# Kernel optimization log

Measured on AMD Instinct MI355X. Metric: run time of the kernel, lower is better.

The kernel has to match this reference:

```python
import jax, jax.numpy as jnp
import numpy as np

NUM_SPECIES = 7
B, A, F = 1024, 48, 384


def setup_inputs() -> dict:
    key = jax.random.key(0)
    ks = jax.random.split(key, 10)
    species = jax.random.randint(ks[0], (B, A), 0, NUM_SPECIES, dtype=jnp.int32)
    aev = jax.random.normal(ks[1], (B, A, F), dtype=jnp.float32)
    def w(k, shape, fan_in):
        s = 1.0 / np.sqrt(fan_in).astype(np.float32)
        return jax.random.uniform(k, shape, jnp.float32, -s, s)
    return {
        "species": species,
        "aev": aev,
        "W1": w(ks[2], (NUM_SPECIES, 256, 384), 384),
        "b1": w(ks[3], (NUM_SPECIES, 256), 384),
        "W2": w(ks[4], (NUM_SPECIES, 192, 256), 256),
        "b2": w(ks[5], (NUM_SPECIES, 192), 256),
        "W3": w(ks[6], (NUM_SPECIES, 160, 192), 192),
        "b3": w(ks[7], (NUM_SPECIES, 160), 192),
        "W4": w(ks[8], (NUM_SPECIES, 1, 160), 160),
        "b4": w(ks[9], (NUM_SPECIES, 1), 160),
    }


def reference(species, aev, W1, b1, W2, b2, W3, b3, W4, b4):
    # species: [B, A] int, aev: [B, A, 384]
    celu = lambda x: jax.nn.celu(x, alpha=0.1)

    def expert(s):
        # Per-species MLP 384->256->192->160->1 applied to all atoms; selected via mask.
        h = celu(jnp.einsum('baf,hf->bah', aev, W1[s]) + b1[s])
        h = celu(jnp.einsum('bah,gh->bag', h, W2[s]) + b2[s])
        h = celu(jnp.einsum('bag,eg->bae', h, W3[s]) + b3[s])
        return (jnp.einsum('bae,oe->bao', h, W4[s]) + b4[s])[..., 0]  # [B, A]

    atom_energy = jnp.zeros(species.shape, aev.dtype)
    for s in range(NUM_SPECIES):  # fixed small expert loop (hard routing)
        atom_energy = jnp.where(species == s, expert(s), atom_energy)
    # scatter-sum atomic energies into per-molecule energies
    return atom_energy.sum(axis=1)  # [B]
```

## Files before the change

kernel.cpp:

```cpp
#include <hip/hip_runtime.h>
#include <math.h>

#define NSPEC 7
#define NMOL 1024
#define APM 48
#define NATOMS (NMOL * APM)
#define FDIM 384

typedef unsigned short u16;
typedef unsigned int u32;
typedef __attribute__((ext_vector_type(8))) short short8;
typedef __attribute__((ext_vector_type(4))) float floatx4;

#define W1_ELEMS_PER_S (16 * 12 * 64 * 8)
#define W2_ELEMS_PER_S (12 * 8 * 64 * 8)
#define W3_ELEMS_PER_S (10 * 6 * 64 * 8)
#define T1 (NSPEC * 16 * 12 * 64)
#define T2 (NSPEC * 12 * 8 * 64)
#define T3 (NSPEC * 10 * 6 * 64)
#define BUCKET_BLOCKS (NATOMS / 256)
#define PACK_BLOCKS ((T1 + T2 + T3) / 256)

#define WS_W1_OFF 32
#define WS_W2_OFF (WS_W1_OFF + 1376256)
#define WS_W3_OFF (WS_W2_OFF + 688128)
#define WS_BKT_OFF (WS_W3_OFF + 430080)

#define BUFST 264

__device__ __forceinline__ float celu01(float x) {
    return x > 0.0f ? x : 0.1f * expm1f(x * 10.0f);
}

__device__ __forceinline__ u16 bfr(float f) {
    u32 u = __float_as_uint(f);
    u += 0x7fffu + ((u >> 16) & 1u);
    return (u16)(u >> 16);
}

__device__ __forceinline__ float bf2f(short s) {
    return __uint_as_float(((u32)(u16)s) << 16);
}

union U8 { short8 v; u16 u[8]; };

__global__ void prep_kernel(const int* __restrict__ species,
                            int* __restrict__ g_cnt, u16* __restrict__ bucket,
                            const float* __restrict__ W1, const float* __restrict__ W2,
                            const float* __restrict__ W3,
                            u16* __restrict__ w1p, u16* __restrict__ w2p,
                            u16* __restrict__ w3p) {
    int t = threadIdx.x;
    if (blockIdx.x < BUCKET_BLOCKS) {
        __shared__ int l_cnt[NSPEC];
        __shared__ int l_base[NSPEC];
        if (t < NSPEC) l_cnt[t] = 0;
        __syncthreads();
        int i = blockIdx.x * 256 + t;
        int s = species[i];
        int lpos = atomicAdd(&l_cnt[s], 1);
        __syncthreads();
        if (t < NSPEC) l_base[t] = atomicAdd(&g_cnt[t], l_cnt[t]);
        __syncthreads();
        bucket[s * NATOMS + l_base[s] + lpos] = (u16)i;
    } else {
        int tid = (blockIdx.x - BUCKET_BLOCKS) * 256 + t;
        const float* W;
        u16* dst;
        int KGS, NTILES, idx;
        if (tid < T1) { W = W1; dst = w1p; KGS = 12; NTILES = 16; idx = tid; }
        else if (tid < T1 + T2) { W = W2; dst = w2p; KGS = 8; NTILES = 12; idx = tid - T1; }
        else { W = W3; dst = w3p; KGS = 6; NTILES = 10; idx = tid - (T1 + T2); }
        int lane = idx & 63;
        int q = idx >> 6;
        int kg = q % KGS; q /= KGS;
        int t2 = q % NTILES;
        int s = q / NTILES;
        int K = KGS * 32;
        int n = t2 * 16 + (lane & 15);
        int k0 = kg * 32 + ((lane >> 4) & 3) * 8;
        const float* src = W + (size_t)(s * NTILES * 16 + n) * K + k0;
        U8 x;
#pragma unroll
        for (int j = 0; j < 8; ++j) x.u[j] = bfr(src[j]);
        *reinterpret_cast<short8*>(dst + (size_t)idx * 8) = x.v;
    }
}

template <int KGS, int NTILES>
__device__ __forceinline__ void run_layer(const short8* af0, const short8* af1,
                                          const u16* __restrict__ wsp,
                                          const float* __restrict__ bias,
                                          u16* __restrict__ outbuf, int lane) {
    const int nl = lane & 15, kg4 = lane >> 4;
    short8 bcur[KGS], bnext[KGS];
    {
        const u16* wb = wsp + (size_t)lane * 8;
#pragma unroll
        for (int kg = 0; kg < KGS; ++kg)
            bcur[kg] = *reinterpret_cast<const short8*>(wb + kg * 512);
    }
#pragma unroll
    for (int t = 0; t < NTILES; ++t) {
        if (t + 1 < NTILES) {
            const u16* wb = wsp + (size_t)((t + 1) * KGS) * 512 + (size_t)lane * 8;
#pragma unroll
            for (int kg = 0; kg < KGS; ++kg)
                bnext[kg] = *reinterpret_cast<const short8*>(wb + kg * 512);
        }
        floatx4 acc0 = {0.f, 0.f, 0.f, 0.f};
        floatx4 acc1 = {0.f, 0.f, 0.f, 0.f};
#pragma unroll
        for (int kg = 0; kg < KGS; ++kg) {
            acc0 = __builtin_amdgcn_mfma_f32_16x16x32_bf16(af0[kg], bcur[kg], acc0, 0, 0, 0);
            acc1 = __builtin_amdgcn_mfma_f32_16x16x32_bf16(af1[kg], bcur[kg], acc1, 0, 0, 0);
        }
        float bn = bias[t * 16 + nl];
#pragma unroll
        for (int r = 0; r < 4; ++r) {
            outbuf[(kg4 * 4 + r) * BUFST + t * 16 + nl] = bfr(celu01(acc0[r] + bn));
            outbuf[(16 + kg4 * 4 + r) * BUFST + t * 16 + nl] = bfr(celu01(acc1[r] + bn));
        }
#pragma unroll
        for (int kg = 0; kg < KGS; ++kg) bcur[kg] = bnext[kg];
    }
}

template <int KGS>
__device__ __forceinline__ void load_a_lds(const u16* __restrict__ buf,
                                           short8* af0, short8* af1, int lane) {
    int nl = lane & 15, kg4 = lane >> 4;
#pragma unroll
    for (int kg = 0; kg < KGS; ++kg) {
        af0[kg] = *reinterpret_cast<const short8*>(buf + (size_t)nl * BUFST + kg * 32 + kg4 * 8);
        af1[kg] = *reinterpret_cast<const short8*>(buf + (size_t)(16 + nl) * BUFST + kg * 32 + kg4 * 8);
    }
}

__global__ __launch_bounds__(128, 2) void mlp_kernel(
    const float* __restrict__ aev,
    const u16* __restrict__ w1p, const u16* __restrict__ w2p, const u16* __restrict__ w3p,
    const float* __restrict__ b1, const float* __restrict__ b2, const float* __restrict__ b3,
    const float* __restrict__ W4, const float* __restrict__ b4,
    const int* __restrict__ g_cnt, const u16* __restrict__ bucket,
    float* __restrict__ out) {
    int s = blockIdx.y;
    int cnt = g_cnt[s];
    int w = threadIdx.x >> 6, lane = threadIdx.x & 63;
    int base = blockIdx.x * 64 + w * 32;
    if (base >= cnt) return;

    __shared__ __align__(16) u16 bufs[2][32 * BUFST];
    u16* buf = &bufs[w][0];

    int nl = lane & 15, kg4 = lane >> 4;

    short8 af0[12], af1[12];
    {
        int i0 = base + nl;       if (i0 >= cnt) i0 = cnt - 1;
        int i1 = base + 16 + nl;  if (i1 >= cnt) i1 = cnt - 1;
        int a0 = (int)bucket[s * NATOMS + i0];
        int a1 = (int)bucket[s * NATOMS + i1];
        const float* ar0 = aev + (size_t)a0 * FDIM;
        const float* ar1 = aev + (size_t)a1 * FDIM;
#pragma unroll
        for (int kg = 0; kg < 12; ++kg) {
            const float4* p0 = (const float4*)(ar0 + kg * 32 + kg4 * 8);
            const float4* p1 = (const float4*)(ar1 + kg * 32 + kg4 * 8);
            float4 a = p0[0], b = p0[1];
            float4 c = p1[0], d = p1[1];
            U8 x, y;
            x.u[0] = bfr(a.x); x.u[1] = bfr(a.y); x.u[2] = bfr(a.z); x.u[3] = bfr(a.w);
            x.u[4] = bfr(b.x); x.u[5] = bfr(b.y); x.u[6] = bfr(b.z); x.u[7] = bfr(b.w);
            y.u[0] = bfr(c.x); y.u[1] = bfr(c.y); y.u[2] = bfr(c.z); y.u[3] = bfr(c.w);
            y.u[4] = bfr(d.x); y.u[5] = bfr(d.y); y.u[6] = bfr(d.z); y.u[7] = bfr(d.w);
            af0[kg] = x.v;
            af1[kg] = y.v;
        }
    }
    run_layer<12, 16>(af0, af1, w1p + (size_t)s * W1_ELEMS_PER_S, b1 + s * 256, buf, lane);

    short8 c0[8], c1[8];
    load_a_lds<8>(buf, c0, c1, lane);
    run_layer<8, 12>(c0, c1, w2p + (size_t)s * W2_ELEMS_PER_S, b2 + s * 192, buf, lane);

    short8 d0[6], d1[6];
    load_a_lds<6>(buf, d0, d1, lane);
    run_layer<6, 10>(d0, d1, w3p + (size_t)s * W3_ELEMS_PER_S, b3 + s * 160, buf, lane);

    {
        int m = lane >> 1, q = lane & 1;
        const u16* h = buf + (size_t)m * BUFST + q * 80;
        const float* w4s = W4 + s * 160 + q * 80;
        float p = 0.f;
#pragma unroll
        for (int c = 0; c < 10; ++c) {
            short8 hv = *reinterpret_cast<const short8*>(h + c * 8);
            const float4* wp4 = (const float4*)(w4s + c * 8);
            float4 wa = wp4[0], wb = wp4[1];
            p += bf2f(hv[0]) * wa.x + bf2f(hv[1]) * wa.y + bf2f(hv[2]) * wa.z + bf2f(hv[3]) * wa.w;
            p += bf2f(hv[4]) * wb.x + bf2f(hv[5]) * wb.y + bf2f(hv[6]) * wb.z + bf2f(hv[7]) * wb.w;
        }
        p += __shfl_down(p, 1, 2);
        int idx = base + m;
        if (q == 0 && idx < cnt) {
            int atom = (int)bucket[s * NATOMS + idx];
            atomicAdd(&out[atom / APM], p + b4[s]);
        }
    }
}

extern "C" void kernel_launch(void* const* d_in, const int* in_sizes, int n_in,
                              void* d_out, int out_size, void* d_ws, size_t ws_size,
                              hipStream_t stream) {
    const int* species = (const int*)d_in[0];
    const float* aev = (const float*)d_in[1];
    const float* W1 = (const float*)d_in[2];
    const float* b1 = (const float*)d_in[3];
    const float* W2 = (const float*)d_in[4];
    const float* b2 = (const float*)d_in[5];
    const float* W3 = (const float*)d_in[6];
    const float* b3 = (const float*)d_in[7];
    const float* W4 = (const float*)d_in[8];
    const float* b4 = (const float*)d_in[9];
    float* out = (float*)d_out;

    unsigned char* wsb = (unsigned char*)d_ws;
    int* g_cnt = (int*)wsb;
    u16* w1p = (u16*)(wsb + WS_W1_OFF);
    u16* w2p = (u16*)(wsb + WS_W2_OFF);
    u16* w3p = (u16*)(wsb + WS_W3_OFF);
    u16* bucket = (u16*)(wsb + WS_BKT_OFF);

    hipMemsetAsync(d_out, 0, NMOL * sizeof(float), stream);
    hipMemsetAsync(g_cnt, 0, 8 * sizeof(int), stream);

    prep_kernel<<<BUCKET_BLOCKS + PACK_BLOCKS, 256, 0, stream>>>(
        species, g_cnt, bucket, W1, W2, W3, w1p, w2p, w3p);

    dim3 grid(NATOMS / 64, NSPEC);
    mlp_kernel<<<grid, 128, 0, stream>>>(aev, w1p, w2p, w3p, b1, b2, b3, W4, b4,
                                         g_cnt, bucket, out);
}
```

Before: 193.4 us.

## Coalesce weight packing via LDS, fold out-zeroing, interleave species grid, deepen prefetch

Weight packing now stages each 16-row tile through LDS with coalesced float4 reads instead of strided per-thread reads. Zeroing of the output is folded into the prep kernel, removing one memset launch. The MLP grid is flattened with species interleaved in the low bits so blocks for different species are scheduled together, and the weight-tile prefetch becomes a configurable multi-buffer (3 deep for layers 2 and 3). CELU switches to the fast __expf form, which may lose some accuracy near zero compared with expm1f, and the deeper buffers raise register pressure.

```diff
diff --git a/kernel.cpp b/kernel.cpp
--- a/kernel.cpp
+++ b/kernel.cpp
@@ -15,11 +15,12 @@
 #define W1_ELEMS_PER_S (16 * 12 * 64 * 8)
 #define W2_ELEMS_PER_S (12 * 8 * 64 * 8)
 #define W3_ELEMS_PER_S (10 * 6 * 64 * 8)
-#define T1 (NSPEC * 16 * 12 * 64)
-#define T2 (NSPEC * 12 * 8 * 64)
-#define T3 (NSPEC * 10 * 6 * 64)
+
 #define BUCKET_BLOCKS (NATOMS / 256)
-#define PACK_BLOCKS ((T1 + T2 + T3) / 256)
+#define PACK1_BLOCKS (NSPEC * 16)
+#define PACK2_BLOCKS (NSPEC * 12)
+#define PACK3_BLOCKS (NSPEC * 10)
+#define PREP_BLOCKS (BUCKET_BLOCKS + PACK1_BLOCKS + PACK2_BLOCKS + PACK3_BLOCKS)
 
 #define WS_W1_OFF 32
 #define WS_W2_OFF (WS_W1_OFF + 1376256)
@@ -29,7 +30,8 @@
 #define BUFST 264
 
 __device__ __forceinline__ float celu01(float x) {
-    return x > 0.0f ? x : 0.1f * expm1f(x * 10.0f);
+    float e = fmaf(0.1f, __expf(x * 10.0f), -0.1f);
+    return x > 0.0f ? x : e;
 }
 
 __device__ __forceinline__ u16 bfr(float f) {
@@ -43,77 +45,97 @@
 }
 
 union U8 { short8 v; u16 u[8]; };
+
+template <int KGS, int NTILES>
+__device__ __forceinline__ void pack_tile(const float* __restrict__ W,
+                                          u16* __restrict__ dst,
+                                          int s, int t2, u16* lds) {
+    const int K = KGS * 32;
+    const int K4 = K / 4;
+    int t = threadIdx.x;
+    const float* wbase = W + ((size_t)(s * NTILES + t2) * 16) * K;
+    for (int i = t; i < 16 * K4; i += 256) {
+        int r = i / K4, c = i % K4;
+        float4 v = ((const float4*)(wbase + (size_t)r * K))[c];
+        u16* d = lds + r * K + c * 4;
+        d[0] = bfr(v.x); d[1] = bfr(v.y); d[2] = bfr(v.z); d[3] = bfr(v.w);
+    }
+    __syncthreads();
+    int w = t >> 6, lane = t & 63;
+    int n = lane & 15, ks = lane >> 4;
+    for (int kg = w; kg < KGS; kg += 4) {
+        short8 v = *reinterpret_cast<const short8*>(lds + n * K + kg * 32 + ks * 8);
+        *reinterpret_cast<short8*>(
+            dst + (((size_t)(s * NTILES + t2) * KGS + kg) * 64 + lane) * 8) = v;
+    }
+}
 
 __global__ void prep_kernel(const int* __restrict__ species,
                             int* __restrict__ g_cnt, u16* __restrict__ bucket,
                             const float* __restrict__ W1, const float* __restrict__ W2,
                             const float* __restrict__ W3,
                             u16* __restrict__ w1p, u16* __restrict__ w2p,
-                            u16* __restrict__ w3p) {
+                            u16* __restrict__ w3p, float* __restrict__ out) {
+    __shared__ u16 lds[16 * 384];
+    __shared__ int l_cnt[NSPEC];
+    __shared__ int l_base[NSPEC];
     int t = threadIdx.x;
-    if (blockIdx.x < BUCKET_BLOCKS) {
-        __shared__ int l_cnt[NSPEC];
-        __shared__ int l_base[NSPEC];
+    int bx = blockIdx.x;
+    if (bx < BUCKET_BLOCKS) {
+        if (bx == 0) {
+            float4 z = {0.f, 0.f, 0.f, 0.f};
+            ((float4*)out)[t] = z;
+        }
         if (t < NSPEC) l_cnt[t] = 0;
         __syncthreads();
-        int i = blockIdx.x * 256 + t;
+        int i = bx * 256 + t;
         int s = species[i];
         int lpos = atomicAdd(&l_cnt[s], 1);
         __syncthreads();
         if (t < NSPEC) l_base[t] = atomicAdd(&g_cnt[t], l_cnt[t]);
         __syncthreads();
         bucket[s * NATOMS + l_base[s] + lpos] = (u16)i;
+    } else if (bx < BUCKET_BLOCKS + PACK1_BLOCKS) {
+        int pid = bx - BUCKET_BLOCKS;
+        pack_tile<12, 16>(W1, w1p, pid / 16, pid % 16, lds);
+    } else if (bx < BUCKET_BLOCKS + PACK1_BLOCKS + PACK2_BLOCKS) {
+        int pid = bx - (BUCKET_BLOCKS + PACK1_BLOCKS);
+        pack_tile<8, 12>(W2, w2p, pid / 12, pid % 12, lds);
     } else {
-        int tid = (blockIdx.x - BUCKET_BLOCKS) * 256 + t;
-        const float* W;
-        u16* dst;
-        int KGS, NTILES, idx;
-        if (tid < T1) { W = W1; dst = w1p; KGS = 12; NTILES = 16; idx = tid; }
-        else if (tid < T1 + T2) { W = W2; dst = w2p; KGS = 8; NTILES = 12; idx = tid - T1; }
-        else { W = W3; dst = w3p; KGS = 6; NTILES = 10; idx = tid - (T1 + T2); }
-        int lane = idx & 63;
-        int q = idx >> 6;
-        int kg = q % KGS; q /= KGS;
-        int t2 = q % NTILES;
-        int s = q / NTILES;
-        int K = KGS * 32;
-        int n = t2 * 16 + (lane & 15);
-        int k0 = kg * 32 + ((lane >> 4) & 3) * 8;
-        const float* src = W + (size_t)(s * NTILES * 16 + n) * K + k0;
-        U8 x;
-#pragma unroll
-        for (int j = 0; j < 8; ++j) x.u[j] = bfr(src[j]);
-        *reinterpret_cast<short8*>(dst + (size_t)idx * 8) = x.v;
-    }
-}
-
-template <int KGS, int NTILES>
+        int pid = bx - (BUCKET_BLOCKS + PACK1_BLOCKS + PACK2_BLOCKS);
+        pack_tile<6, 10>(W3, w3p, pid / 10, pid % 10, lds);
+    }
+}
+
+template <int KGS, int NT, int NBUF>
 __device__ __forceinline__ void run_layer(const short8* af0, const short8* af1,
                                           const u16* __restrict__ wsp,
                                           const float* __restrict__ bias,
                                           u16* __restrict__ outbuf, int lane) {
     const int nl = lane & 15, kg4 = lane >> 4;
-    short8 bcur[KGS], bnext[KGS];
-    {
-        const u16* wb = wsp + (size_t)lane * 8;
+    const u16* wb = wsp + (size_t)lane * 8;
+    short8 b[NBUF][KGS];
+#pragma unroll
+    for (int p = 0; p < NBUF - 1; ++p)
 #pragma unroll
         for (int kg = 0; kg < KGS; ++kg)
-            bcur[kg] = *reinterpret_cast<const short8*>(wb + kg * 512);
-    }
-#pragma unroll
-    for (int t = 0; t < NTILES; ++t) {
-        if (t + 1 < NTILES) {
-            const u16* wb = wsp + (size_t)((t + 1) * KGS) * 512 + (size_t)lane * 8;
+            b[p][kg] = *reinterpret_cast<const short8*>(wb + ((size_t)p * KGS + kg) * 512);
+#pragma unroll
+    for (int t = 0; t < NT; ++t) {
+        int pre = t + NBUF - 1;
+        if (pre < NT) {
+            int slot = pre % NBUF;
 #pragma unroll
             for (int kg = 0; kg < KGS; ++kg)
-                bnext[kg] = *reinterpret_cast<const short8*>(wb + kg * 512);
-        }
+                b[slot][kg] = *reinterpret_cast<const short8*>(wb + ((size_t)pre * KGS + kg) * 512);
+        }
+        int cur = t % NBUF;
         floatx4 acc0 = {0.f, 0.f, 0.f, 0.f};
         floatx4 acc1 = {0.f, 0.f, 0.f, 0.f};
 #pragma unroll
         for (int kg = 0; kg < KGS; ++kg) {
-            acc0 = __builtin_amdgcn_mfma_f32_16x16x32_bf16(af0[kg], bcur[kg], acc0, 0, 0, 0);
-            acc1 = __builtin_amdgcn_mfma_f32_16x16x32_bf16(af1[kg], bcur[kg], acc1, 0, 0, 0);
+            acc0 = __builtin_amdgcn_mfma_f32_16x16x32_bf16(af0[kg], b[cur][kg], acc0, 0, 0, 0);
+            acc1 = __builtin_amdgcn_mfma_f32_16x16x32_bf16(af1[kg], b[cur][kg], acc1, 0, 0, 0);
         }
         float bn = bias[t * 16 + nl];
 #pragma unroll
@@ -121,8 +143,6 @@
             outbuf[(kg4 * 4 + r) * BUFST + t * 16 + nl] = bfr(celu01(acc0[r] + bn));
             outbuf[(16 + kg4 * 4 + r) * BUFST + t * 16 + nl] = bfr(celu01(acc1[r] + bn));
         }
-#pragma unroll
-        for (int kg = 0; kg < KGS; ++kg) bcur[kg] = bnext[kg];
     }
 }
 
@@ -144,10 +164,13 @@
     const float* __restrict__ W4, const float* __restrict__ b4,
     const int* __restrict__ g_cnt, const u16* __restrict__ bucket,
     float* __restrict__ out) {
-    int s = blockIdx.y;
+    int bx = blockIdx.x;
+    int s = bx & 7;
+    if (s >= NSPEC) return;
+    int chunk = bx >> 3;
     int cnt = g_cnt[s];
     int w = threadIdx.x >> 6, lane = threadIdx.x & 63;
-    int base = blockIdx.x * 64 + w * 32;
+    int base = chunk * 64 + w * 32;
     if (base >= cnt) return;
 
     __shared__ __align__(16) u16 bufs[2][32 * BUFST];
@@ -178,15 +201,15 @@
             af1[kg] = y.v;
         }
     }
-    run_layer<12, 16>(af0, af1, w1p + (size_t)s * W1_ELEMS_PER_S, b1 + s * 256, buf, lane);
+    run_layer<12, 16, 2>(af0, af1, w1p + (size_t)s * W1_ELEMS_PER_S, b1 + s * 256, buf, lane);
 
     short8 c0[8], c1[8];
     load_a_lds<8>(buf, c0, c1, lane);
-    run_layer<8, 12>(c0, c1, w2p + (size_t)s * W2_ELEMS_PER_S, b2 + s * 192, buf, lane);
+    run_layer<8, 12, 3>(c0, c1, w2p + (size_t)s * W2_ELEMS_PER_S, b2 + s * 192, buf, lane);
 
     short8 d0[6], d1[6];
     load_a_lds<6>(buf, d0, d1, lane);
-    run_layer<6, 10>(d0, d1, w3p + (size_t)s * W3_ELEMS_PER_S, b3 + s * 160, buf, lane);
+    run_layer<6, 10, 3>(d0, d1, w3p + (size_t)s * W3_ELEMS_PER_S, b3 + s * 160, buf, lane);
 
     {
         int m = lane >> 1, q = lane & 1;
@@ -232,13 +255,11 @@
     u16* w3p = (u16*)(wsb + WS_W3_OFF);
     u16* bucket = (u16*)(wsb + WS_BKT_OFF);
 
-    hipMemsetAsync(d_out, 0, NMOL * sizeof(float), stream);
     hipMemsetAsync(g_cnt, 0, 8 * sizeof(int), stream);
 
-    prep_kernel<<<BUCKET_BLOCKS + PACK_BLOCKS, 256, 0, stream>>>(
-        species, g_cnt, bucket, W1, W2, W3, w1p, w2p, w3p);
-
-    dim3 grid(NATOMS / 64, NSPEC);
-    mlp_kernel<<<grid, 128, 0, stream>>>(aev, w1p, w2p, w3p, b1, b2, b3, W4, b4,
-                                         g_cnt, bucket, out);
-}
+    prep_kernel<<<PREP_BLOCKS, 256, 0, stream>>>(
+        species, g_cnt, bucket, W1, W2, W3, w1p, w2p, w3p, out);
+
+    mlp_kernel<<<8 * (NATOMS / 64), 128, 0, stream>>>(
+        aev, w1p, w2p, w3p, b1, b2, b3, W4, b4, g_cnt, bucket, out);
+}
```

Result: faster. 163.5 us (-15.5%).
